# Optimization experiments

Measured on AMD Instinct MI355X. Metric: run time of the kernel, lower is better.

## Reference

```python
import jax, jax.numpy as jnp
import numpy as np

# Config mirroring init_kwargs
B, N, DM = 16, 512, 512          # batch, max_ast_len, hidden_size
PAR_HEADS, BRO_HEADS = 4, 4
H = PAR_HEADS + BRO_HEADS        # 8 heads
DK = DM // H                     # 64
R = 8                            # max_rel_pos
L = 2                            # num_layers
DFF = 4 * DM
EPS = 1e-5


def setup_inputs() -> dict:
    key = jax.random.key(0)
    ks = jax.random.split(key, 24)
    s = 0.02
    inp = {
        "src_emb": jax.random.normal(ks[0], (B, N, DM), jnp.float32),
        "par_edges": jax.random.randint(ks[1], (B, R, N), 0, N, jnp.int32),
        "bro_edges": jax.random.randint(ks[2], (B, R, N), 0, N, jnp.int32),
        # relative-position embedding tables (par heads ++ bro heads along head axis,
        # exactly what concat_vec(rel_par_*, rel_bro_*, dim=1) produces): [H, R, DK]
        "rel_q": s * jax.random.normal(ks[3], (H, R, DK), jnp.float32),
        "rel_k": s * jax.random.normal(ks[4], (H, R, DK), jnp.float32),
        "rel_v": s * jax.random.normal(ks[5], (H, R, DK), jnp.float32),
        # per-layer weights, stacked over layers
        "Wq": s * jax.random.normal(ks[6], (L, DM, DM), jnp.float32),
        "Wk": s * jax.random.normal(ks[7], (L, DM, DM), jnp.float32),
        "Wv": s * jax.random.normal(ks[8], (L, DM, DM), jnp.float32),
        "Wo": s * jax.random.normal(ks[9], (L, DM, DM), jnp.float32),
        "ln1_g": jnp.ones((L, DM), jnp.float32),
        "ln1_b": jnp.zeros((L, DM), jnp.float32),
        "W1": s * jax.random.normal(ks[10], (L, DM, DFF), jnp.float32),
        "b1": jnp.zeros((L, DFF), jnp.float32),
        "W2": s * jax.random.normal(ks[11], (L, DFF, DM), jnp.float32),
        "b2": jnp.zeros((L, DM), jnp.float32),
        "ln2_g": jnp.ones((L, DM), jnp.float32),
        "ln2_b": jnp.zeros((L, DM), jnp.float32),
        "normf_g": jnp.ones((DM,), jnp.float32),
        "normf_b": jnp.zeros((DM,), jnp.float32),
    }
    return inp


def _ln(x, g, b):
    m = x.mean(-1, keepdims=True)
    v = ((x - m) ** 2).mean(-1, keepdims=True)
    return (x - m) * jax.lax.rsqrt(v + EPS) * g + b


def _gather_nodes(t, idx):
    # t: [B,H,N,DK], idx: [B,H,R,N,1] -> [B,H,R,N,DK] gathered along node axis
    t_b = jnp.broadcast_to(t[:, :, None], (B, H, R, N, DK))
    return jnp.take_along_axis(t_b, idx, axis=3)


def _forward(src_emb, rel_q, rel_k, rel_v, Wq, Wk, Wv, Wo, ln1_g, ln1_b,
             W1, b1, W2, b2, ln2_g, ln2_b, normf_g, normf_b,
             par_edges, bro_edges):
    # start_nodes = concat_pos: repeat par edges over par heads, bro over bro heads
    start = jnp.concatenate(
        [jnp.repeat(par_edges[:, None], PAR_HEADS, axis=1),
         jnp.repeat(bro_edges[:, None], BRO_HEADS, axis=1)], axis=1)  # [B,H,R,N]
    idx = start[..., None].astype(jnp.int32)  # [B,H,R,N,1]
    scale = 1.0 / np.sqrt(DK)
    x = src_emb
    for i in range(L):
        q = (x @ Wq[i]).reshape(B, N, H, DK).transpose(0, 2, 1, 3)  # bhnd
        k = (x @ Wk[i]).reshape(B, N, H, DK).transpose(0, 2, 1, 3)
        v = (x @ Wv[i]).reshape(B, N, H, DK).transpose(0, 2, 1, 3)
        k_s = _gather_nodes(k, idx)  # [B,H,R,N,DK]
        v_s = _gather_nodes(v, idx)
        # Shaw-style relational scores over the R sparse neighbors only
        scores = (jnp.einsum('bhnd,bhrnd->bhrn', q, k_s)
                  + jnp.einsum('bhnd,hrd->bhrn', q, rel_k)
                  + jnp.einsum('hrd,bhrnd->bhrn', rel_q, k_s)) * scale
        attn = jax.nn.softmax(scores, axis=2)  # softmax over relative positions
        ctx = (jnp.einsum('bhrn,bhrnd->bhnd', attn, v_s)
               + jnp.einsum('bhrn,hrd->bhnd', attn, rel_v))
        ctx = ctx.transpose(0, 2, 1, 3).reshape(B, N, DM)
        x = _ln(x + ctx @ Wo[i], ln1_g[i], ln1_b[i])
        ff = jax.nn.relu(x @ W1[i] + b1[i]) @ W2[i] + b2[i]
        x = _ln(x + ff, ln2_g[i], ln2_b[i])
    return _ln(x, normf_g, normf_b)  # final self.norm


def reference(src_emb, par_edges, bro_edges, rel_q, rel_k, rel_v,
              Wq, Wk, Wv, Wo, ln1_g, ln1_b, W1, b1, W2, b2,
              ln2_g, ln2_b, normf_g, normf_b):
    return _forward(src_emb, rel_q, rel_k, rel_v, Wq, Wk, Wv, Wo,
                    ln1_g, ln1_b, W1, b1, W2, b2, ln2_g, ln2_b,
                    normf_g, normf_b, par_edges, bro_edges)
```

## Files before the change

### kernel.cpp

```cpp
#include <hip/hip_runtime.h>
#include <hip/hip_bf16.h>


#define BB 16
#define NN 512
#define DMM 512
#define HH 8
#define DKK 64
#define RR 8
#define LL 2
#define DFFV 2048
#define PAR_HEADS 4
#define EPSV 1e-5f

typedef __bf16 bf16x8 __attribute__((ext_vector_type(8)));
typedef float f32x4 __attribute__((ext_vector_type(4)));

__device__ __forceinline__ unsigned short f2bf(float f) {
    unsigned u = __float_as_uint(f);
    u += 0x7fff + ((u >> 16) & 1);
    return (unsigned short)(u >> 16);
}
__device__ __forceinline__ float bf2f(unsigned short u) {
    return __uint_as_float(((unsigned)u) << 16);
}

__global__ __launch_bounds__(256) void transpose_qkvo_kernel(
    const float* __restrict__ Wq, const float* __restrict__ Wk,
    const float* __restrict__ Wv, const float* __restrict__ Wo,
    unsigned short* __restrict__ wqkvT, unsigned short* __restrict__ woT)
{
    __shared__ float tile[32][33];
    int layer = blockIdx.z >> 2, which = blockIdx.z & 3;
    const float* s = (which == 0 ? Wq : which == 1 ? Wk : which == 2 ? Wv : Wo)
                     + (size_t)layer * DMM * DMM;
    unsigned short* d = (which < 3)
        ? wqkvT + (size_t)layer * 1536 * DMM + (size_t)which * DMM * DMM
        : woT + (size_t)layer * DMM * DMM;
    int k0 = blockIdx.y * 32, n0 = blockIdx.x * 32;
    int tx = threadIdx.x & 31, ty = threadIdx.x >> 5;
#pragma unroll
    for (int i = 0; i < 4; ++i)
        tile[ty + i * 8][tx] = s[(size_t)(k0 + ty + i * 8) * DMM + (n0 + tx)];
    __syncthreads();
#pragma unroll
    for (int i = 0; i < 4; ++i)
        d[(size_t)(n0 + ty + i * 8) * DMM + (k0 + tx)] = f2bf(tile[tx][ty + i * 8]);
}

__global__ __launch_bounds__(256) void transpose_w_kernel(
    const float* __restrict__ src, unsigned short* __restrict__ dst,
    int K, int N, size_t zStride)
{
    __shared__ float tile[32][33];
    const float* s = src + (size_t)blockIdx.z * K * N;
    unsigned short* d = dst + (size_t)blockIdx.z * zStride;
    int k0 = blockIdx.y * 32, n0 = blockIdx.x * 32;
    int tx = threadIdx.x & 31, ty = threadIdx.x >> 5;
#pragma unroll
    for (int i = 0; i < 4; ++i)
        tile[ty + i * 8][tx] = s[(size_t)(k0 + ty + i * 8) * N + (n0 + tx)];
    __syncthreads();
#pragma unroll
    for (int i = 0; i < 4; ++i)
        d[(size_t)(n0 + ty + i * 8) * K + (k0 + tx)] = f2bf(tile[tx][ty + i * 8]);
}

__global__ __launch_bounds__(256) void convert_x_kernel(
    const float* __restrict__ src, float* __restrict__ x, unsigned short* __restrict__ xb, int n4)
{
    int i = blockIdx.x * blockDim.x + threadIdx.x;
    int stride = gridDim.x * blockDim.x;
    for (; i < n4; i += stride) {
        float4 f = ((const float4*)src)[i];
        ((float4*)x)[i] = f;
        ushort4 u;
        u.x = f2bf(f.x); u.y = f2bf(f.y); u.z = f2bf(f.z); u.w = f2bf(f.w);
        ((ushort4*)xb)[i] = u;
    }
}

template<bool OUTBF, bool DORELU>
__global__ __launch_bounds__(256) void gemm_kernel(
    const unsigned short* __restrict__ A,
    const unsigned short* __restrict__ Bt,
    float* __restrict__ Cf,
    unsigned short* __restrict__ Cb,
    const float* __restrict__ bias,
    int M, int N, int K, int kLen)
{
    constexpr int BM = 128, BN = 64, BK = 64;
    __shared__ __align__(16) unsigned short As[BM * BK];
    __shared__ __align__(16) unsigned short Bs[BN * BK];
    int tid = threadIdx.x, lane = tid & 63, w = tid >> 6;
    int wr = w >> 1, wc = w & 1;

    int gx = gridDim.x;
    int nwg = gx * gridDim.y;
    int flat = blockIdx.x + gx * blockIdx.y;
    int qq = nwg >> 3;
    int swz = (flat & 7) * qq + (flat >> 3);
    int bx = swz % gx, by = swz / gx;
    int mBase = by * BM, nBase = bx * BN;
    int kStart = blockIdx.z * kLen;

    f32x4 acc[4][2];
#pragma unroll
    for (int i = 0; i < 4; ++i)
#pragma unroll
        for (int j = 0; j < 2; ++j) acc[i][j] = (f32x4){0.f, 0.f, 0.f, 0.f};

    for (int k0 = kStart; k0 < kStart + kLen; k0 += BK) {
#pragma unroll
        for (int it = 0; it < 4; ++it) {
            int i = it * 256 + tid;
            int row = i >> 3, slot = i & 7;
            int gcol = (slot ^ (row & 7)) * 8;
            const unsigned short* ga = A + (size_t)(mBase + row) * K + k0 + gcol;
            __builtin_amdgcn_global_load_lds(
                (const __attribute__((address_space(1))) void*)ga,
                (__attribute__((address_space(3))) void*)(As + i * 8), 16, 0, 0);
        }
#pragma unroll
        for (int it = 0; it < 2; ++it) {
            int i = it * 256 + tid;
            int row = i >> 3, slot = i & 7;
            int gcol = (slot ^ (row & 7)) * 8;
            const unsigned short* gb = Bt + (size_t)(nBase + row) * K + k0 + gcol;
            __builtin_amdgcn_global_load_lds(
                (const __attribute__((address_space(1))) void*)gb,
                (__attribute__((address_space(3))) void*)(Bs + i * 8), 16, 0, 0);
        }
        __syncthreads();

        int rsel = lane & 15, g0 = lane >> 4;
        bf16x8 a[4][2], b[2][2];
#pragma unroll
        for (int m = 0; m < 4; ++m) {
            int row = wr * 64 + m * 16 + rsel;
#pragma unroll
            for (int ks = 0; ks < 2; ++ks) {
                int s = (g0 + ks * 4) ^ (row & 7);
                a[m][ks] = *(const bf16x8*)((const char*)As + row * 128 + s * 16);
            }
        }
#pragma unroll
        for (int n = 0; n < 2; ++n) {
            int row = wc * 32 + n * 16 + rsel;
#pragma unroll
            for (int ks = 0; ks < 2; ++ks) {
                int s = (g0 + ks * 4) ^ (row & 7);
                b[n][ks] = *(const bf16x8*)((const char*)Bs + row * 128 + s * 16);
            }
        }
#pragma unroll
        for (int m = 0; m < 4; ++m)
#pragma unroll
            for (int n = 0; n < 2; ++n)
#pragma unroll
                for (int ks = 0; ks < 2; ++ks)
                    acc[m][n] = __builtin_amdgcn_mfma_f32_16x16x32_bf16(a[m][ks], b[n][ks], acc[m][n], 0, 0, 0);
        __syncthreads();
    }

    size_t zoff = (size_t)blockIdx.z * M * N;
    int rbase = (lane >> 4) * 4;
    int cloc = lane & 15;
#pragma unroll
    for (int m = 0; m < 4; ++m) {
#pragma unroll
        for (int n = 0; n < 2; ++n) {
            int col = nBase + wc * 32 + n * 16 + cloc;
            float bv = bias ? bias[col] : 0.0f;
#pragma unroll
            for (int j = 0; j < 4; ++j) {
                int row = mBase + wr * 64 + m * 16 + rbase + j;
                float val = acc[m][n][j] + bv;
                if (DORELU) val = fmaxf(val, 0.0f);
                if (OUTBF) Cb[zoff + (size_t)row * N + col] = f2bf(val);
                else       Cf[zoff + (size_t)row * N + col] = val;
            }
        }
    }
}

__global__ __launch_bounds__(256) void attn_kernel(
    const unsigned short* __restrict__ qkv,
    const int* __restrict__ par, const int* __restrict__ bro,
    const float* __restrict__ relq, const float* __restrict__ relk,
    const float* __restrict__ relv, unsigned short* __restrict__ cb)
{
    int wid = blockIdx.x * 4 + (threadIdx.x >> 6);
    int lane = threadIdx.x & 63;
    int n = wid & (NN - 1);
    int t = wid >> 9;
    int h = t & (HH - 1);
    int b = t >> 3;
    const int* edges = (h < PAR_HEADS) ? par : bro;

    float qd = bf2f(qkv[(size_t)(b * NN + n) * 1536 + h * DKK + lane]);
    float s[RR];
    int e[RR];
#pragma unroll
    for (int r = 0; r < RR; ++r) {
        e[r] = edges[(b * RR + r) * NN + n];
        float kd = bf2f(qkv[(size_t)(b * NN + e[r]) * 1536 + DMM + h * DKK + lane]);
        float rkd = relk[(h * RR + r) * DKK + lane];
        float rqd = relq[(h * RR + r) * DKK + lane];
        float tp = qd * kd + qd * rkd + rqd * kd;
#pragma unroll
        for (int off = 32; off > 0; off >>= 1) tp += __shfl_xor(tp, off, 64);
        s[r] = tp;
    }
    const float scale = 0.125f;
    float mx = -1e30f;
#pragma unroll
    for (int r = 0; r < RR; ++r) { s[r] *= scale; mx = fmaxf(mx, s[r]); }
    float denom = 0.f;
#pragma unroll
    for (int r = 0; r < RR; ++r) { s[r] = __expf(s[r] - mx); denom += s[r]; }
    float inv = 1.0f / denom;
    float od = 0.f;
#pragma unroll
    for (int r = 0; r < RR; ++r) {
        float vd = bf2f(qkv[(size_t)(b * NN + e[r]) * 1536 + 2 * DMM + h * DKK + lane]);
        float rvd = relv[(h * RR + r) * DKK + lane];
        od += s[r] * (vd + rvd);
    }
    od *= inv;
    cb[(size_t)(b * NN + n) * DMM + h * DKK + lane] = f2bf(od);
}

__global__ __launch_bounds__(256) void ln_kernel(
    const float* __restrict__ xin, const float* __restrict__ add0,
    const float* __restrict__ add1, const float* __restrict__ bias,
    float* __restrict__ xout, unsigned short* __restrict__ xbout,
    const float* __restrict__ g, const float* __restrict__ bb)
{
    int row = blockIdx.x * 4 + (threadIdx.x >> 6);
    int lane = threadIdx.x & 63;
    const float* xr = xin + (size_t)row * DMM;
    const float* a0 = add0 ? add0 + (size_t)row * DMM : nullptr;
    const float* a1 = add1 ? add1 + (size_t)row * DMM : nullptr;
    float vals[8];
    float s = 0.f;
#pragma unroll
    for (int j = 0; j < 8; ++j) {
        int c = lane + j * 64;
        float t = xr[c];
        if (a0) t += a0[c];
        if (a1) t += a1[c];
        if (bias) t += bias[c];
        vals[j] = t;
        s += t;
    }
#pragma unroll
    for (int off = 32; off > 0; off >>= 1) s += __shfl_xor(s, off, 64);
    float mean = s * (1.0f / DMM);
    float s2 = 0.f;
#pragma unroll
    for (int j = 0; j < 8; ++j) { float d = vals[j] - mean; s2 += d * d; }
#pragma unroll
    for (int off = 32; off > 0; off >>= 1) s2 += __shfl_xor(s2, off, 64);
    float inv = rsqrtf(s2 * (1.0f / DMM) + EPSV);
#pragma unroll
    for (int j = 0; j < 8; ++j) {
        int c = lane + j * 64;
        float y = (vals[j] - mean) * inv * g[c] + bb[c];
        xout[(size_t)row * DMM + c] = y;
        if (xbout) xbout[(size_t)row * DMM + c] = f2bf(y);
    }
}

extern "C" void kernel_launch(void* const* d_in, const int* in_sizes, int n_in,
                              void* d_out, int out_size, void* d_ws, size_t ws_size,
                              hipStream_t stream)
{
    const float* src_emb = (const float*)d_in[0];
    const int*   par     = (const int*)d_in[1];
    const int*   bro     = (const int*)d_in[2];
    const float* rel_q   = (const float*)d_in[3];
    const float* rel_k   = (const float*)d_in[4];
    const float* rel_v   = (const float*)d_in[5];
    const float* Wq      = (const float*)d_in[6];
    const float* Wk      = (const float*)d_in[7];
    const float* Wv      = (const float*)d_in[8];
    const float* Wo      = (const float*)d_in[9];
    const float* ln1_g   = (const float*)d_in[10];
    const float* ln1_b   = (const float*)d_in[11];
    const float* W1      = (const float*)d_in[12];
    const float* b1      = (const float*)d_in[13];
    const float* W2      = (const float*)d_in[14];
    const float* b2      = (const float*)d_in[15];
    const float* ln2_g   = (const float*)d_in[16];
    const float* ln2_b   = (const float*)d_in[17];
    const float* normf_g = (const float*)d_in[18];
    const float* normf_b = (const float*)d_in[19];

    const size_t MB = 1024 * 1024;
    const int M = BB * NN;
    char* ws = (char*)d_ws;
    float*          p    = (float*)(ws + 0 * MB);
    unsigned short* qkvb = (unsigned short*)(ws + 0 * MB);
    unsigned short* h1   = (unsigned short*)(ws + 32 * MB);
    unsigned short* xb   = (unsigned short*)(ws + 64 * MB);
    unsigned short* cbuf = (unsigned short*)(ws + 72 * MB);
    unsigned short* wqkvT = (unsigned short*)(ws + 80 * MB);
    unsigned short* woT  = wqkvT + (size_t)LL * 1536 * DMM;
    unsigned short* w1T  = woT + (size_t)LL * DMM * DMM;
    unsigned short* w2T  = w1T + (size_t)LL * DMM * DFFV;
    float* p0 = p;
    float* p1 = p + (size_t)M * DMM;
    float* x = (float*)d_out;

    transpose_qkvo_kernel<<<dim3(16, 16, LL * 4), 256, 0, stream>>>(
        Wq, Wk, Wv, Wo, wqkvT, woT);
    transpose_w_kernel<<<dim3(DFFV / 32, DMM / 32, LL), 256, 0, stream>>>(
        W1, w1T, DMM, DFFV, (size_t)DMM * DFFV);
    transpose_w_kernel<<<dim3(DMM / 32, DFFV / 32, LL), 256, 0, stream>>>(
        W2, w2T, DFFV, DMM, (size_t)DMM * DFFV);

    convert_x_kernel<<<2048, 256, 0, stream>>>(src_emb, x, xb, M * DMM / 4);

    for (int l = 0; l < LL; ++l) {
        const unsigned short* wqkv_l = wqkvT + (size_t)l * 1536 * DMM;
        const unsigned short* wo_l = woT + (size_t)l * DMM * DMM;
        const unsigned short* w1_l = w1T + (size_t)l * DMM * DFFV;
        const unsigned short* w2_l = w2T + (size_t)l * DFFV * DMM;

        gemm_kernel<true, false><<<dim3(1536 / 64, M / 128, 1), 256, 0, stream>>>(
            xb, wqkv_l, nullptr, qkvb, nullptr, M, 1536, DMM, DMM);

        attn_kernel<<<BB * HH * NN / 4, 256, 0, stream>>>(qkvb, par, bro,
                                                          rel_q, rel_k, rel_v, cbuf);

        gemm_kernel<false, false><<<dim3(512 / 64, M / 128, 2), 256, 0, stream>>>(
            cbuf, wo_l, p, nullptr, nullptr, M, DMM, DMM, DMM / 2);
        ln_kernel<<<M / 4, 256, 0, stream>>>(x, p0, p1, nullptr, x, xb,
                                             ln1_g + l * DMM, ln1_b + l * DMM);

        gemm_kernel<true, true><<<dim3(DFFV / 64, M / 128, 1), 256, 0, stream>>>(
            xb, w1_l, nullptr, h1, b1 + l * DFFV, M, DFFV, DMM, DMM);
        gemm_kernel<false, false><<<dim3(512 / 64, M / 128, 2), 256, 0, stream>>>(
            h1, w2_l, p, nullptr, nullptr, M, DMM, DFFV, DFFV / 2);
        ln_kernel<<<M / 4, 256, 0, stream>>>(x, p0, p1, b2 + l * DMM, x, xb,
                                             ln2_g + l * DMM, ln2_b + l * DMM);
    }

    ln_kernel<<<M / 4, 256, 0, stream>>>(x, nullptr, nullptr, nullptr, x, nullptr,
                                         normf_g, normf_b);
}
```

Baseline: 436.7 us.

## Double-buffer GEMM LDS tiles and restructure sparse attention per wave

The GEMM kernel now keeps two LDS buffers and issues the next K-tile's global-to-LDS loads before computing the current one, waiting with partial vmcnt so that loads overlap the MFMA work. The attention kernel is rewritten so that each wave handles 8 nodes. It hoists the relative embeddings into registers, loads all edge indices with one coalesced load, and replaces eight full-wave reductions per node with a transpose-style butterfly reduction that leaves each score in its own lane. Blocks are mapped so that each XCD works on a subset of batches, for better L2 locality. The double buffering doubles LDS use per block, which may lower occupancy.

```diff
diff --git a/kernel.cpp b/kernel.cpp
--- a/kernel.cpp
+++ b/kernel.cpp
@@ -90,8 +90,8 @@
     int M, int N, int K, int kLen)
 {
     constexpr int BM = 128, BN = 64, BK = 64;
-    __shared__ __align__(16) unsigned short As[BM * BK];
-    __shared__ __align__(16) unsigned short Bs[BN * BK];
+    __shared__ __align__(16) unsigned short As[2][BM * BK];
+    __shared__ __align__(16) unsigned short Bs[2][BN * BK];
     int tid = threadIdx.x, lane = tid & 63, w = tid >> 6;
     int wr = w >> 1, wc = w & 1;
 
@@ -104,34 +104,47 @@
     int mBase = by * BM, nBase = bx * BN;
     int kStart = blockIdx.z * kLen;
 
+    const unsigned short* gA = A + (size_t)mBase * K;
+    const unsigned short* gB = Bt + (size_t)nBase * K;
+
     f32x4 acc[4][2];
 #pragma unroll
     for (int i = 0; i < 4; ++i)
 #pragma unroll
         for (int j = 0; j < 2; ++j) acc[i][j] = (f32x4){0.f, 0.f, 0.f, 0.f};
 
-    for (int k0 = kStart; k0 < kStart + kLen; k0 += BK) {
+    auto stage = [&](int buf, int k0) {
 #pragma unroll
         for (int it = 0; it < 4; ++it) {
             int i = it * 256 + tid;
             int row = i >> 3, slot = i & 7;
             int gcol = (slot ^ (row & 7)) * 8;
-            const unsigned short* ga = A + (size_t)(mBase + row) * K + k0 + gcol;
             __builtin_amdgcn_global_load_lds(
-                (const __attribute__((address_space(1))) void*)ga,
-                (__attribute__((address_space(3))) void*)(As + i * 8), 16, 0, 0);
+                (const __attribute__((address_space(1))) void*)(gA + (size_t)row * K + k0 + gcol),
+                (__attribute__((address_space(3))) void*)(As[buf] + i * 8), 16, 0, 0);
         }
 #pragma unroll
         for (int it = 0; it < 2; ++it) {
             int i = it * 256 + tid;
             int row = i >> 3, slot = i & 7;
             int gcol = (slot ^ (row & 7)) * 8;
-            const unsigned short* gb = Bt + (size_t)(nBase + row) * K + k0 + gcol;
             __builtin_amdgcn_global_load_lds(
-                (const __attribute__((address_space(1))) void*)gb,
-                (__attribute__((address_space(3))) void*)(Bs + i * 8), 16, 0, 0);
-        }
-        __syncthreads();
+                (const __attribute__((address_space(1))) void*)(gB + (size_t)row * K + k0 + gcol),
+                (__attribute__((address_space(3))) void*)(Bs[buf] + i * 8), 16, 0, 0);
+        }
+    };
+
+    int nt = kLen / BK;
+    stage(0, kStart);
+    int cur = 0;
+    for (int t = 0; t < nt; ++t) {
+        if (t + 1 < nt) {
+            stage(cur ^ 1, kStart + (t + 1) * BK);
+            asm volatile("s_waitcnt vmcnt(6)" ::: "memory");
+        } else {
+            asm volatile("s_waitcnt vmcnt(0)" ::: "memory");
+        }
+        __builtin_amdgcn_s_barrier();
 
         int rsel = lane & 15, g0 = lane >> 4;
         bf16x8 a[4][2], b[2][2];
@@ -141,7 +154,7 @@
 #pragma unroll
             for (int ks = 0; ks < 2; ++ks) {
                 int s = (g0 + ks * 4) ^ (row & 7);
-                a[m][ks] = *(const bf16x8*)((const char*)As + row * 128 + s * 16);
+                a[m][ks] = *(const bf16x8*)((const char*)As[cur] + row * 128 + s * 16);
             }
         }
 #pragma unroll
@@ -150,7 +163,7 @@
 #pragma unroll
             for (int ks = 0; ks < 2; ++ks) {
                 int s = (g0 + ks * 4) ^ (row & 7);
-                b[n][ks] = *(const bf16x8*)((const char*)Bs + row * 128 + s * 16);
+                b[n][ks] = *(const bf16x8*)((const char*)Bs[cur] + row * 128 + s * 16);
             }
         }
 #pragma unroll
@@ -160,7 +173,8 @@
 #pragma unroll
                 for (int ks = 0; ks < 2; ++ks)
                     acc[m][n] = __builtin_amdgcn_mfma_f32_16x16x32_bf16(a[m][ks], b[n][ks], acc[m][n], 0, 0, 0);
-        __syncthreads();
+        __builtin_amdgcn_s_barrier();
+        cur ^= 1;
     }
 
     size_t zoff = (size_t)blockIdx.z * M * N;
@@ -190,45 +204,90 @@
     const float* __restrict__ relq, const float* __restrict__ relk,
     const float* __restrict__ relv, unsigned short* __restrict__ cb)
 {
-    int wid = blockIdx.x * 4 + (threadIdx.x >> 6);
+    int f = blockIdx.x;
+    int xcd = f & 7;
+    int j = f >> 3;
+    int b = xcd + 8 * (j & 1);
+    int rem = j >> 1;
+    int h = rem >> 4;
+    int n0 = (rem & 15) * 32;
+    int w = threadIdx.x >> 6;
     int lane = threadIdx.x & 63;
-    int n = wid & (NN - 1);
-    int t = wid >> 9;
-    int h = t & (HH - 1);
-    int b = t >> 3;
+    int nw = n0 + w * 8;
+
+    float rq[RR], rk[RR], rv[RR];
+#pragma unroll
+    for (int r = 0; r < RR; ++r) {
+        rq[r] = relq[(h * RR + r) * DKK + lane];
+        rk[r] = relk[(h * RR + r) * DKK + lane];
+        rv[r] = relv[(h * RR + r) * DKK + lane];
+    }
     const int* edges = (h < PAR_HEADS) ? par : bro;
-
-    float qd = bf2f(qkv[(size_t)(b * NN + n) * 1536 + h * DKK + lane]);
-    float s[RR];
-    int e[RR];
-#pragma unroll
-    for (int r = 0; r < RR; ++r) {
-        e[r] = edges[(b * RR + r) * NN + n];
-        float kd = bf2f(qkv[(size_t)(b * NN + e[r]) * 1536 + DMM + h * DKK + lane]);
-        float rkd = relk[(h * RR + r) * DKK + lane];
-        float rqd = relq[(h * RR + r) * DKK + lane];
-        float tp = qd * kd + qd * rkd + rqd * kd;
-#pragma unroll
-        for (int off = 32; off > 0; off >>= 1) tp += __shfl_xor(tp, off, 64);
-        s[r] = tp;
-    }
-    const float scale = 0.125f;
-    float mx = -1e30f;
-#pragma unroll
-    for (int r = 0; r < RR; ++r) { s[r] *= scale; mx = fmaxf(mx, s[r]); }
-    float denom = 0.f;
-#pragma unroll
-    for (int r = 0; r < RR; ++r) { s[r] = __expf(s[r] - mx); denom += s[r]; }
-    float inv = 1.0f / denom;
-    float od = 0.f;
-#pragma unroll
-    for (int r = 0; r < RR; ++r) {
-        float vd = bf2f(qkv[(size_t)(b * NN + e[r]) * 1536 + 2 * DMM + h * DKK + lane]);
-        float rvd = relv[(h * RR + r) * DKK + lane];
-        od += s[r] * (vd + rvd);
-    }
-    od *= inv;
-    cb[(size_t)(b * NN + n) * DMM + h * DKK + lane] = f2bf(od);
+    int e_all = edges[(b * RR + (lane & 7)) * NN + nw + (lane >> 3)];
+
+    const unsigned short* qrow = qkv + (size_t)b * NN * 1536 + h * DKK;
+
+#pragma unroll
+    for (int nl = 0; nl < 8; ++nl) {
+        int n = nw + nl;
+        float qd = bf2f(qrow[(size_t)n * 1536 + lane]);
+        float t[RR];
+        int e[RR];
+#pragma unroll
+        for (int r = 0; r < RR; ++r) {
+            int er = __builtin_amdgcn_readlane(e_all, nl * 8 + r);
+            e[r] = er;
+            float kd = bf2f(qkv[(size_t)(b * NN + er) * 1536 + DMM + h * DKK + lane]);
+            t[r] = kd * (qd + rq[r]) + qd * rk[r];
+        }
+        {
+            bool hb = lane & 4;
+#pragma unroll
+            for (int rr = 0; rr < 4; ++rr) {
+                float send = hb ? t[rr] : t[rr + 4];
+                float keep = hb ? t[rr + 4] : t[rr];
+                t[rr] = keep + __shfl_xor(send, 4, 64);
+            }
+        }
+        {
+            bool hb = lane & 2;
+#pragma unroll
+            for (int rr = 0; rr < 2; ++rr) {
+                float send = hb ? t[rr] : t[rr + 2];
+                float keep = hb ? t[rr + 2] : t[rr];
+                t[rr] = keep + __shfl_xor(send, 2, 64);
+            }
+        }
+        {
+            bool hb = lane & 1;
+            float send = hb ? t[0] : t[1];
+            float keep = hb ? t[1] : t[0];
+            t[0] = keep + __shfl_xor(send, 1, 64);
+        }
+        float s = t[0];
+        s += __shfl_xor(s, 8, 64);
+        s += __shfl_xor(s, 16, 64);
+        s += __shfl_xor(s, 32, 64);
+        s *= 0.125f;
+        float mx = s;
+        mx = fmaxf(mx, __shfl_xor(mx, 1, 64));
+        mx = fmaxf(mx, __shfl_xor(mx, 2, 64));
+        mx = fmaxf(mx, __shfl_xor(mx, 4, 64));
+        float ee = __expf(s - mx);
+        float den = ee;
+        den += __shfl_xor(den, 1, 64);
+        den += __shfl_xor(den, 2, 64);
+        den += __shfl_xor(den, 4, 64);
+        float a = ee / den;
+        float od = 0.f;
+#pragma unroll
+        for (int r = 0; r < RR; ++r) {
+            float ar = __shfl(a, (lane & 56) | r, 64);
+            float vd = bf2f(qkv[(size_t)(b * NN + e[r]) * 1536 + 2 * DMM + h * DKK + lane]);
+            od = fmaf(ar, vd + rv[r], od);
+        }
+        cb[(size_t)(b * NN + n) * DMM + h * DKK + lane] = f2bf(od);
+    }
 }
 
 __global__ __launch_bounds__(256) void ln_kernel(
@@ -331,8 +390,7 @@
         gemm_kernel<true, false><<<dim3(1536 / 64, M / 128, 1), 256, 0, stream>>>(
             xb, wqkv_l, nullptr, qkvb, nullptr, M, 1536, DMM, DMM);
 
-        attn_kernel<<<BB * HH * NN / 4, 256, 0, stream>>>(qkvb, par, bro,
-                                                          rel_q, rel_k, rel_v, cbuf);
+        attn_kernel<<<2048, 256, 0, stream>>>(qkvb, par, bro, rel_q, rel_k, rel_v, cbuf);
 
         gemm_kernel<false, false><<<dim3(512 / 64, M / 128, 2), 256, 0, stream>>>(
             cbuf, wo_l, p, nullptr, nullptr, M, DMM, DMM, DMM / 2);
```

Result: slower. 456.8 us (+4.6%).
